# Performance work log

Measured on AMD Instinct MI355X. Metric: run time of the kernel, lower is better.

## Reference

```python
import jax, jax.numpy as jnp
import numpy as np

NEG = jnp.float32(-1e30)  # finite stand-in for -inf in masked max
SLOPE = 0.01              # F.leaky_relu default negative slope


def _lrelu(v):
    return jnp.where(v >= 0, v, SLOPE * v)


def _mlp(pts, w1, b1, w2, b2, w3, b3):
    # pts: [2, N] -> [64, N]; 1x1 Conv1d == pointwise linear over channel dim
    z = _lrelu(w1 @ pts + b1[:, None])
    z = _lrelu(w2 @ z + b2[:, None])
    z = _lrelu(w3 @ z + b3[:, None])
    return z


def setup_inputs() -> dict:
    key = jax.random.key(0)
    ks = jax.random.split(key, 10)
    B, C, H, W = 4, 19, 256, 256
    x = jax.random.randint(ks[0], (B, C, H, W), 0, 2, dtype=jnp.int32)
    # grid exactly as in the torch module: meshgrid of two linspaces, flattened
    g = np.array(np.meshgrid(np.linspace(-1, 1, 256), np.linspace(-1, 1, 256),
                             sparse=False)).astype(np.float32)  # [2,256,256]
    grid = jnp.asarray(g.reshape(2, -1))  # [2, 65536]
    w1 = jax.random.normal(ks[1], (64, 2), jnp.float32) * 0.5
    b1 = jax.random.normal(ks[2], (64,), jnp.float32) * 0.1
    w2 = jax.random.normal(ks[3], (64, 64), jnp.float32) * 0.125
    b2 = jax.random.normal(ks[4], (64,), jnp.float32) * 0.1
    w3 = jax.random.normal(ks[5], (64, 64), jnp.float32) * 0.125
    b3 = jax.random.normal(ks[6], (64,), jnp.float32) * 0.1
    fcw = jax.random.normal(ks[7], (512, 64 * C), jnp.float32)
    fcb = jax.random.normal(ks[8], (512,), jnp.float32) * 0.1
    return {"x": x, "grid": grid, "w1": w1, "b1": b1, "w2": w2, "b2": b2,
            "w3": w3, "b3": b3, "fcw": fcw, "fcb": fcb}


def reference(x, grid, w1, b1, w2, b2, w3, b3, fcw, fcb):
    B, C = x.shape[0], x.shape[1]
    # Pointwise MLP on the shared grid once (grid identical for all b,c)
    feats = _mlp(grid, w1, b1, w2, b2, w3, b3)                 # [64, N]
    # Fallback feature for empty masks: MLP on a single zero point
    zero_feat = _mlp(jnp.zeros((2, 1), feats.dtype),
                     w1, b1, w2, b2, w3, b3)[:, 0]             # [64]
    mask = (x.reshape(B, C, -1) == 1)                          # [B, C, N]
    # Masked max over the ragged point sets, fully vectorized
    masked = jnp.where(mask[:, :, None, :], feats[None, None], NEG)
    z = jnp.max(masked, axis=-1)                               # [B, C, 64]
    empty = ~jnp.any(mask, axis=-1)                            # [B, C]
    z = jnp.where(empty[..., None], zero_feat, z)
    flat = z.reshape(B, C * 64)                                # channel-major cat
    # EqualLinear: weight scaled by 1/sqrt(in_dim) (lr_mul=1)
    scale = jnp.float32(1.0 / np.sqrt(C * 64))
    out = flat @ (fcw * scale).T + fcb                         # [B, 512]
    return jnp.repeat(out[:, None, :], 18, axis=1)             # [B, 18, 512]
```

## Files before the change

### kernel.cpp

```cpp
#include <hip/hip_runtime.h>

#define NPTS  65536
#define NBC   76
#define NREP  8
#define KEYN  4864

typedef _Float16 f16;
typedef __fp16   h16x2 __attribute__((ext_vector_type(2)));
typedef _Float16 f16x8 __attribute__((ext_vector_type(8)));
typedef float    f32x4 __attribute__((ext_vector_type(4)));

__device__ __forceinline__ float lrelu(float v) { return fmaxf(v, 0.01f * v); }

__device__ __forceinline__ unsigned pkrtz(float lo, float hi) {
  h16x2 p = __builtin_amdgcn_cvt_pkrtz(lo, hi);
  return __builtin_bit_cast(unsigned, p);
}
__device__ __forceinline__ unsigned pkey(unsigned u) {
  unsigned t = (u >> 15) & 0x00010001u;
  return u ^ (0x80008000u | (t * 0x7FFFu));
}
__device__ __forceinline__ unsigned pkmax(unsigned a, unsigned b) {
  unsigned d;
  asm("v_pk_max_u16 %0, %1, %2" : "=v"(d) : "v"(a), "v"(b));
  return d;
}
__device__ __forceinline__ unsigned sext1(unsigned x, int b) {
  return (unsigned)(((int)(x << (31 - b))) >> 31);
}

__global__ __launch_bounds__(512, 8) void k1_fused(
    const int* __restrict__ x, const float* __restrict__ grid,
    const float* __restrict__ w1, const float* __restrict__ b1,
    const float* __restrict__ w2, const float* __restrict__ b2,
    const float* __restrict__ w3, const float* __restrict__ b3,
    unsigned* __restrict__ keys)
{
  __shared__ __align__(16) unsigned char smem[36864];
  __shared__ unsigned long long mbits[NBC];
  f16* zA  = (f16*)(smem);
  f16* zB  = (f16*)(smem + 9216);
  f16* wf2 = (f16*)(smem + 18432);
  f16* wf3 = (f16*)(smem + 27648);
  unsigned* zkey = (unsigned*)(smem + 18432);

  const int t    = threadIdx.x;
  const int lane = t & 63;
  const int wv   = t >> 6;
  const int n0   = blockIdx.x * 64;

  int xv[10];
  #pragma unroll
  for (int i = 0; i < 10; ++i) {
    int bc = wv + 8 * i;
    xv[i] = (bc < NBC) ? x[(bc << 16) + n0 + lane] : 0;
  }

  {
    int ch = t >> 3, k0 = (t & 7) * 8;
    const float4* s2 = (const float4*)(w2 + ch * 64 + k0);
    float4 a = s2[0], b = s2[1];
    *(uint4*)&wf2[ch * 72 + k0] =
        make_uint4(pkrtz(a.x, a.y), pkrtz(a.z, a.w), pkrtz(b.x, b.y), pkrtz(b.z, b.w));
    const float4* s3 = (const float4*)(w3 + ch * 64 + k0);
    float4 c = s3[0], d = s3[1];
    *(uint4*)&wf3[ch * 72 + k0] =
        make_uint4(pkrtz(c.x, c.y), pkrtz(c.z, c.w), pkrtz(d.x, d.y), pkrtz(d.z, d.w));
  }

  {
    float g0 = grid[n0 + lane], g1 = grid[NPTS + n0 + lane];
    unsigned uo[4];
    #pragma unroll
    for (int p = 0; p < 4; ++p) {
      int j = wv * 8 + p * 2;
      float z0 = lrelu(w1[2 * j] * g0 + w1[2 * j + 1] * g1 + b1[j]);
      float z1 = lrelu(w1[2 * j + 2] * g0 + w1[2 * j + 3] * g1 + b1[j + 1]);
      uo[p] = pkrtz(z0, z1);
    }
    *(uint4*)&zA[lane * 72 + wv * 8] = make_uint4(uo[0], uo[1], uo[2], uo[3]);
  }
  __syncthreads();

  const int chb = (wv & 3) * 16, pth = (wv >> 2) * 32;
  const int c15 = lane & 15, q = lane >> 4;
  const int chq = chb + q * 4;
  const int pt0 = pth + c15, pt1 = pth + 16 + c15;

  f32x4 acc0, acc1;

  {
    float4 bias = *(const float4*)(b2 + chq);
    acc0 = (f32x4){bias.x, bias.y, bias.z, bias.w};
    acc1 = acc0;
    #pragma unroll
    for (int k0 = 0; k0 < 64; k0 += 32) {
      f16x8 af = *(const f16x8*)&wf2[(chb + c15) * 72 + k0 + q * 8];
      f16x8 b0 = *(const f16x8*)&zA[pt0 * 72 + k0 + q * 8];
      f16x8 b1f = *(const f16x8*)&zA[pt1 * 72 + k0 + q * 8];
      acc0 = __builtin_amdgcn_mfma_f32_16x16x32_f16(af, b0, acc0, 0, 0, 0);
      acc1 = __builtin_amdgcn_mfma_f32_16x16x32_f16(af, b1f, acc1, 0, 0, 0);
    }
    *(uint2*)&zB[pt0 * 72 + chq] =
        make_uint2(pkrtz(lrelu(acc0[0]), lrelu(acc0[1])),
                   pkrtz(lrelu(acc0[2]), lrelu(acc0[3])));
    *(uint2*)&zB[pt1 * 72 + chq] =
        make_uint2(pkrtz(lrelu(acc1[0]), lrelu(acc1[1])),
                   pkrtz(lrelu(acc1[2]), lrelu(acc1[3])));
  }

  #pragma unroll
  for (int i = 0; i < 10; ++i) {
    int bc = wv + 8 * i;
    unsigned long long m = __ballot(xv[i] == 1);
    if (bc < NBC && lane == 0) mbits[bc] = m;
  }
  __syncthreads();

  {
    float4 bias = *(const float4*)(b3 + chq);
    acc0 = (f32x4){bias.x, bias.y, bias.z, bias.w};
    acc1 = acc0;
    #pragma unroll
    for (int k0 = 0; k0 < 64; k0 += 32) {
      f16x8 af = *(const f16x8*)&wf3[(chb + c15) * 72 + k0 + q * 8];
      f16x8 b0 = *(const f16x8*)&zB[pt0 * 72 + k0 + q * 8];
      f16x8 b1f = *(const f16x8*)&zB[pt1 * 72 + k0 + q * 8];
      acc0 = __builtin_amdgcn_mfma_f32_16x16x32_f16(af, b0, acc0, 0, 0, 0);
      acc1 = __builtin_amdgcn_mfma_f32_16x16x32_f16(af, b1f, acc1, 0, 0, 0);
    }
    int r0 = chq >> 1;
    zkey[r0 * 68 + pt0]       = pkey(pkrtz(lrelu(acc0[0]), lrelu(acc0[1])));
    zkey[(r0 + 1) * 68 + pt0] = pkey(pkrtz(lrelu(acc0[2]), lrelu(acc0[3])));
    zkey[r0 * 68 + pt1]       = pkey(pkrtz(lrelu(acc1[0]), lrelu(acc1[1])));
    zkey[(r0 + 1) * 68 + pt1] = pkey(pkrtz(lrelu(acc1[2]), lrelu(acc1[3])));
  }
  __syncthreads();

  const int rw = t & 31, bg = t >> 5;
  const int bc0 = bg * 5;

  unsigned mlo[5], mhi[5], uacc[5];
  #pragma unroll
  for (int ii = 0; ii < 5; ++ii) {
    int bc = bc0 + ii;
    unsigned long long m = (bc < NBC) ? mbits[bc] : 0ull;
    mlo[ii] = (unsigned)m;
    mhi[ii] = (unsigned)(m >> 32);
    uacc[ii] = 0u;
  }

  #pragma unroll
  for (int np = 0; np < 16; ++np) {
    uint4 z4 = *(const uint4*)&zkey[rw * 68 + np * 4];
    const int p = np * 4, pb = p & 31;
    #pragma unroll
    for (int ii = 0; ii < 5; ++ii) {
      unsigned m = (p < 32) ? mlo[ii] : mhi[ii];
      unsigned s0 = sext1(m, pb),     s1 = sext1(m, pb + 1);
      unsigned s2 = sext1(m, pb + 2), s3 = sext1(m, pb + 3);
      unsigned a = uacc[ii];
      a = pkmax(a, z4.x & s0); a = pkmax(a, z4.y & s1);
      a = pkmax(a, z4.z & s2); a = pkmax(a, z4.w & s3);
      uacc[ii] = a;
    }
  }

  unsigned* krep = keys + (blockIdx.x & (NREP - 1)) * KEYN;
  #pragma unroll
  for (int ii = 0; ii < 5; ++ii) {
    int bc = bc0 + ii;
    if (bc < NBC) {
      unsigned lo = uacc[ii] & 0xFFFFu, hi = uacc[ii] >> 16;
      if (lo) atomicMax(&krep[bc * 64 + 2 * rw], lo);
      if (hi) atomicMax(&krep[bc * 64 + 2 * rw + 1], hi);
    }
  }
}

__global__ __launch_bounds__(256) void k2_fc(
    const unsigned* __restrict__ keys,
    const float* __restrict__ b1, const float* __restrict__ w2,
    const float* __restrict__ b2, const float* __restrict__ w3,
    const float* __restrict__ b3,
    const float* __restrict__ fcw, const float* __restrict__ fcb,
    float* __restrict__ out)
{
  __shared__ float flat[4864];
  __shared__ float za[64], zb[64], zf[64];
  const int t = threadIdx.x;

  if (t < 64) za[t] = lrelu(b1[t]);
  __syncthreads();
  if (t < 64) {
    float s = b2[t];
    #pragma unroll 8
    for (int k = 0; k < 64; ++k) s += w2[t * 64 + k] * za[k];
    zb[t] = lrelu(s);
  }
  __syncthreads();
  if (t < 64) {
    float s = b3[t];
    #pragma unroll 8
    for (int k = 0; k < 64; ++k) s += w3[t * 64 + k] * zb[k];
    zf[t] = lrelu(s);
  }
  __syncthreads();

  for (int idx = t; idx < 4864; idx += 256) {
    unsigned m = keys[idx];
    #pragma unroll
    for (int r = 1; r < NREP; ++r) m = max(m, keys[r * KEYN + idx]);
    float v;
    if (m) {
      unsigned u = (m & 0x8000u) ? (m ^ 0x8000u) : (~m & 0xFFFFu);
      unsigned short us = (unsigned short)u;
      v = (float)__builtin_bit_cast(f16, us);
    } else {
      v = zf[idx & 63];
    }
    flat[idx] = v;
  }
  __syncthreads();

  const int wv = t >> 6, lane = t & 63;
  const int o = blockIdx.x * 4 + wv;
  const float* wrow = fcw + o * 1216;
  float fa0 = 0.f, fa1 = 0.f, fa2 = 0.f, fa3 = 0.f;
  #pragma unroll
  for (int i = 0; i < 19; ++i) {
    int jj = i * 64 + lane;
    float wvv = wrow[jj];
    fa0 += wvv * flat[jj];
    fa1 += wvv * flat[1216 + jj];
    fa2 += wvv * flat[2432 + jj];
    fa3 += wvv * flat[3648 + jj];
  }
  #pragma unroll
  for (int off = 32; off > 0; off >>= 1) {
    fa0 += __shfl_xor(fa0, off);
    fa1 += __shfl_xor(fa1, off);
    fa2 += __shfl_xor(fa2, off);
    fa3 += __shfl_xor(fa3, off);
  }
  const float scale = 0.028676966733820225f;
  float cb = fcb[o];
  if (lane < 18) {
    out[(0 * 18 + lane) * 512 + o] = fa0 * scale + cb;
    out[(1 * 18 + lane) * 512 + o] = fa1 * scale + cb;
    out[(2 * 18 + lane) * 512 + o] = fa2 * scale + cb;
    out[(3 * 18 + lane) * 512 + o] = fa3 * scale + cb;
  }
}

extern "C" void kernel_launch(void* const* d_in, const int* in_sizes, int n_in,
                              void* d_out, int out_size, void* d_ws, size_t ws_size,
                              hipStream_t stream)
{
  const int*   x    = (const int*)d_in[0];
  const float* grid = (const float*)d_in[1];
  const float* w1   = (const float*)d_in[2];
  const float* b1   = (const float*)d_in[3];
  const float* w2   = (const float*)d_in[4];
  const float* b2   = (const float*)d_in[5];
  const float* w3   = (const float*)d_in[6];
  const float* b3   = (const float*)d_in[7];
  const float* fcw  = (const float*)d_in[8];
  const float* fcb  = (const float*)d_in[9];
  float* out = (float*)d_out;

  unsigned* keys = (unsigned*)d_ws;

  (void)hipMemsetAsync(d_ws, 0, NREP * KEYN * sizeof(unsigned), stream);
  hipLaunchKernelGGL(k1_fused, dim3(1024), dim3(512), 0, stream,
                     x, grid, w1, b1, w2, b2, w3, b3, keys);
  hipLaunchKernelGGL(k2_fc, dim3(128), dim3(256), 0, stream,
                     keys, b1, w2, b2, w3, b3, fcw, fcb, out);
}
```

Baseline: 129.8 us.

## Split fused MLP and masked-max kernel into two kernels via global key buffer

Splits the fused kernel in two. The first computes the per-point MLP features and writes packed keys to a global scratch buffer. The second loads the mask bits from x, stages those keys into shared memory and does the masked max. The likely aim is to shrink the MLP kernel's register and shared-memory footprint so that occupancy and latency hiding improve. The cost is an extra kernel launch and a global round trip of 8 MB of keys.

```diff
diff --git a/kernel.cpp b/kernel.cpp
--- a/kernel.cpp
+++ b/kernel.cpp
@@ -29,32 +29,25 @@
   return (unsigned)(((int)(x << (31 - b))) >> 31);
 }
 
-__global__ __launch_bounds__(512, 8) void k1_fused(
-    const int* __restrict__ x, const float* __restrict__ grid,
+__global__ __launch_bounds__(512, 8) void kA_mlp(
+    const float* __restrict__ grid,
     const float* __restrict__ w1, const float* __restrict__ b1,
     const float* __restrict__ w2, const float* __restrict__ b2,
     const float* __restrict__ w3, const float* __restrict__ b3,
-    unsigned* __restrict__ keys)
+    unsigned* __restrict__ kbuf)
 {
   __shared__ __align__(16) unsigned char smem[36864];
-  __shared__ unsigned long long mbits[NBC];
   f16* zA  = (f16*)(smem);
   f16* zB  = (f16*)(smem + 9216);
   f16* wf2 = (f16*)(smem + 18432);
   f16* wf3 = (f16*)(smem + 27648);
-  unsigned* zkey = (unsigned*)(smem + 18432);
 
   const int t    = threadIdx.x;
   const int lane = t & 63;
   const int wv   = t >> 6;
   const int n0   = blockIdx.x * 64;
 
-  int xv[10];
-  #pragma unroll
-  for (int i = 0; i < 10; ++i) {
-    int bc = wv + 8 * i;
-    xv[i] = (bc < NBC) ? x[(bc << 16) + n0 + lane] : 0;
-  }
+  float g0 = grid[n0 + lane], g1 = grid[NPTS + n0 + lane];
 
   {
     int ch = t >> 3, k0 = (t & 7) * 8;
@@ -69,7 +62,6 @@
   }
 
   {
-    float g0 = grid[n0 + lane], g1 = grid[NPTS + n0 + lane];
     unsigned uo[4];
     #pragma unroll
     for (int p = 0; p < 4; ++p) {
@@ -108,13 +100,6 @@
         make_uint2(pkrtz(lrelu(acc1[0]), lrelu(acc1[1])),
                    pkrtz(lrelu(acc1[2]), lrelu(acc1[3])));
   }
-
-  #pragma unroll
-  for (int i = 0; i < 10; ++i) {
-    int bc = wv + 8 * i;
-    unsigned long long m = __ballot(xv[i] == 1);
-    if (bc < NBC && lane == 0) mbits[bc] = m;
-  }
   __syncthreads();
 
   {
@@ -129,11 +114,43 @@
       acc0 = __builtin_amdgcn_mfma_f32_16x16x32_f16(af, b0, acc0, 0, 0, 0);
       acc1 = __builtin_amdgcn_mfma_f32_16x16x32_f16(af, b1f, acc1, 0, 0, 0);
     }
+    unsigned* kb = kbuf + (unsigned)blockIdx.x * 2048;
     int r0 = chq >> 1;
-    zkey[r0 * 68 + pt0]       = pkey(pkrtz(lrelu(acc0[0]), lrelu(acc0[1])));
-    zkey[(r0 + 1) * 68 + pt0] = pkey(pkrtz(lrelu(acc0[2]), lrelu(acc0[3])));
-    zkey[r0 * 68 + pt1]       = pkey(pkrtz(lrelu(acc1[0]), lrelu(acc1[1])));
-    zkey[(r0 + 1) * 68 + pt1] = pkey(pkrtz(lrelu(acc1[2]), lrelu(acc1[3])));
+    kb[r0 * 64 + pt0]       = pkey(pkrtz(lrelu(acc0[0]), lrelu(acc0[1])));
+    kb[(r0 + 1) * 64 + pt0] = pkey(pkrtz(lrelu(acc0[2]), lrelu(acc0[3])));
+    kb[r0 * 64 + pt1]       = pkey(pkrtz(lrelu(acc1[0]), lrelu(acc1[1])));
+    kb[(r0 + 1) * 64 + pt1] = pkey(pkrtz(lrelu(acc1[2]), lrelu(acc1[3])));
+  }
+}
+
+__global__ __launch_bounds__(512, 8) void kB_max(
+    const int* __restrict__ x, const unsigned* __restrict__ kbuf,
+    unsigned* __restrict__ keys)
+{
+  __shared__ unsigned zk[32 * 68];
+  __shared__ unsigned long long mbits[NBC];
+
+  const int t    = threadIdx.x;
+  const int lane = t & 63;
+  const int wv   = t >> 6;
+  const int n0   = blockIdx.x * 64;
+
+  const uint4 kv = *(const uint4*)(kbuf + (unsigned)blockIdx.x * 2048 + t * 4);
+
+  int xv[10];
+  #pragma unroll
+  for (int i = 0; i < 10; ++i) {
+    int bc = wv + 8 * i;
+    xv[i] = (bc < NBC) ? x[(bc << 16) + n0 + lane] : 0;
+  }
+
+  *(uint4*)&zk[(t >> 4) * 68 + (t & 15) * 4] = kv;
+
+  #pragma unroll
+  for (int i = 0; i < 10; ++i) {
+    int bc = wv + 8 * i;
+    unsigned long long m = __ballot(xv[i] == 1);
+    if (bc < NBC && lane == 0) mbits[bc] = m;
   }
   __syncthreads();
 
@@ -152,7 +169,7 @@
 
   #pragma unroll
   for (int np = 0; np < 16; ++np) {
-    uint4 z4 = *(const uint4*)&zkey[rw * 68 + np * 4];
+    uint4 z4 = *(const uint4*)&zk[rw * 68 + np * 4];
     const int p = np * 4, pb = p & 31;
     #pragma unroll
     for (int ii = 0; ii < 5; ++ii) {
@@ -270,10 +287,13 @@
   float* out = (float*)d_out;
 
   unsigned* keys = (unsigned*)d_ws;
+  unsigned* kbuf = (unsigned*)d_ws + 65536;
 
   (void)hipMemsetAsync(d_ws, 0, NREP * KEYN * sizeof(unsigned), stream);
-  hipLaunchKernelGGL(k1_fused, dim3(1024), dim3(512), 0, stream,
-                     x, grid, w1, b1, w2, b2, w3, b3, keys);
+  hipLaunchKernelGGL(kA_mlp, dim3(1024), dim3(512), 0, stream,
+                     grid, w1, b1, w2, b2, w3, b3, kbuf);
+  hipLaunchKernelGGL(kB_max, dim3(1024), dim3(512), 0, stream,
+                     x, kbuf, keys);
   hipLaunchKernelGGL(k2_fc, dim3(128), dim3(256), 0, stream,
                      keys, b1, w2, b2, w3, b3, fcw, fcb, out);
 }
```

Measured after the change: 132.7 us. 1.02x slower.
